# Optimization experiments

Measured on AMD Instinct MI355X. Metric: run time of the kernel, lower is better.

The kernel has to match this reference:

```python
import jax, jax.numpy as jnp
import numpy as np


def axisangle2mat(p):
    # p: [N, 6] = (rotation vector rx,ry,rz, translation tx,ty,tz) -> [N, 3, 4]
    v = p[:, :3]
    t = p[:, 3:]
    theta = jnp.sqrt(jnp.sum(v * v, axis=-1) + 1e-12)  # [N]
    k = v / theta[:, None]
    kx, ky, kz = k[:, 0], k[:, 1], k[:, 2]
    zero = jnp.zeros_like(kx)
    K = jnp.stack([
        jnp.stack([zero, -kz, ky], -1),
        jnp.stack([kz, zero, -kx], -1),
        jnp.stack([-ky, kx, zero], -1),
    ], -2)  # [N,3,3]
    I = jnp.eye(3, dtype=p.dtype)
    s = jnp.sin(theta)[:, None, None]
    c = (1.0 - jnp.cos(theta))[:, None, None]
    R = I + s * K + c * jnp.matmul(K, K)
    return jnp.concatenate([R, t[:, :, None]], axis=-1)  # [N,3,4]


def grid_sample_3d(vol, grid):
    # vol: [D,H,W]; grid: [...,3] with last dim (x,y,z) in [-1,1].
    # Replicates F.grid_sample(mode='bilinear', padding_mode='zeros', align_corners=False).
    D, H, W = vol.shape
    ix = ((grid[..., 0] + 1.0) * W - 1.0) * 0.5
    iy = ((grid[..., 1] + 1.0) * H - 1.0) * 0.5
    iz = ((grid[..., 2] + 1.0) * D - 1.0) * 0.5
    x0 = jnp.floor(ix); y0 = jnp.floor(iy); z0 = jnp.floor(iz)
    fx = ix - x0; fy = iy - y0; fz = iz - z0
    vol_flat = vol.reshape(-1)
    out = jnp.zeros(grid.shape[:-1], vol.dtype)
    for dz in (0, 1):
        for dy in (0, 1):
            for dx in (0, 1):
                xc = x0 + dx; yc = y0 + dy; zc = z0 + dz
                wgt = ((fx if dx else 1.0 - fx) * (fy if dy else 1.0 - fy) * (fz if dz else 1.0 - fz))
                valid = ((xc >= 0) & (xc < W) & (yc >= 0) & (yc < H) & (zc >= 0) & (zc < D))
                xi = jnp.clip(xc, 0, W - 1).astype(jnp.int32)
                yi = jnp.clip(yc, 0, H - 1).astype(jnp.int32)
                zi = jnp.clip(zc, 0, D - 1).astype(jnp.int32)
                v = vol_flat[(zi * H + yi) * W + xi]
                out = out + jnp.where(valid, v * wgt, 0.0)
    return out


def setup_inputs() -> dict:
    key = jax.random.key(0)
    ks = jax.random.split(key, 8)
    B, n, D, H, W = 4096, 2048, 256, 256, 256
    x = jax.random.normal(ks[0], (1, 1, D, H, W), dtype=jnp.float32)
    # voxel-space sample points inside the volume
    sampleGrid = jax.random.uniform(ks[1], (B, 3), dtype=jnp.float32) * jnp.array([W - 1, H - 1, D - 1], jnp.float32)
    ax = jnp.concatenate([
        jax.random.normal(ks[2], (B, 1, 3), dtype=jnp.float32) * 0.1,   # small rotations
        jax.random.normal(ks[3], (B, 1, 3), dtype=jnp.float32) * 5.0,   # translations (voxels)
    ], axis=-1)
    low = jax.random.uniform(ks[4], (B, 1, 3), dtype=jnp.float32) * 2.0
    ext = jax.random.uniform(ks[5], (B, 1, 3), dtype=jnp.float32) * 4.0 + 1.0
    bound = jnp.concatenate([low, low + ext], axis=1)  # [B,2,3], bound[:,1] > bound[:,0]
    A = jax.random.normal(ks[6], (B, 3, 3), dtype=jnp.float32) * 0.3
    InvCovScaled = jnp.einsum('bij,bkj->bik', A, A) + 0.5 * jnp.eye(3, dtype=jnp.float32)  # SPD
    xyz_psf = jax.random.normal(ks[7], (B, n, 3), dtype=jnp.float32)
    psf_sigma = jnp.ones((1,), jnp.float32)  # unused in forward (as in the original)
    return dict(x=x, sampleGrid=sampleGrid, ax=ax, bound=bound,
                InvCovScaled=InvCovScaled, psf_sigma=psf_sigma, xyz_psf=xyz_psf)


def reference(x, sampleGrid, ax, bound, InvCovScaled, psf_sigma, xyz_psf):
    # x: [1,1,D,H,W]; sampleGrid: [B,3]; ax: [B,1,6]; bound: [B,2,3];
    # InvCovScaled: [B,3,3]; xyz_psf: [B,n,3] (the torch.randn draw, made explicit)
    W = x.shape[-1]; H = x.shape[-2]; D = x.shape[-3]
    size = (W, H, D)  # matches torch: size = [x.shape[-1], x.shape[-2], x.shape[-3]]
    scaled_xyz_psf = 2.0 * jax.nn.sigmoid(xyz_psf) - 1.0                      # [B,n,3]
    half = (bound[:, 1, :] - bound[:, 0, :]) * 0.5                            # [B,3]
    bound_psf = scaled_xyz_psf * half[:, None]                                # [B,n,3]
    mat = axisangle2mat(ax.reshape(-1, 6)).reshape(ax.shape[:-1] + (3, 4))    # [B,1,3,4]
    R = mat[:, 0, :, :3]                                                      # [B,3,3]
    T = mat[:, 0, :, 3]                                                       # [B,3]
    # trans_first=True: R @ (p + T)
    mat_sampleGrid = jnp.einsum('bij,bj->bi', R, sampleGrid + T)[:, None]     # [B,1,3]
    psf_sampleGrid = mat_sampleGrid + bound_psf                               # [B,n,3]
    norm = jnp.array([size[0] - 1, size[1] - 1, size[2] - 1], psf_sampleGrid.dtype)
    grid = 2.0 * (psf_sampleGrid / norm - 0.5)
    psf_x = grid_sample_3d(x[0, 0], grid)                                     # [B,n]
    # Mahalanobis-style weights: exp(-0.5 * c^T InvCov c)
    q = jnp.einsum('bni,bij,bnj->bn', bound_psf, InvCovScaled, bound_psf)
    w = jnp.exp(-0.5 * q)                                                     # [B,n]
    y = jnp.sum(psf_x * w, axis=-1) / jnp.sum(w, axis=-1)                     # [B]
    return y
```

## Files before the change

kernel.cpp:

```cpp
#include <hip/hip_runtime.h>
#include <math.h>

constexpr int NT   = 256;
constexpr int WPB  = 4;
constexpr int DIMV = 256;
constexpr int RS   = 8;
constexpr int RROW = 9;
constexpr int RSLICE = RS * RROW;

__device__ __forceinline__ float rflf(float x) {
    return __uint_as_float(__builtin_amdgcn_readfirstlane(__float_as_uint(x)));
}
__device__ __forceinline__ float fexp2(float x) {
#if __has_builtin(__builtin_amdgcn_exp2f)
    return __builtin_amdgcn_exp2f(x);
#else
    return __expf(x * 0.6931471805599453f);
#endif
}

__global__ __launch_bounds__(NT, 4) void psf_sample_kernel(
    const float* __restrict__ vol,
    const float* __restrict__ sampleGrid,
    const float* __restrict__ ax,
    const float* __restrict__ bound,
    const float* __restrict__ invcov,
    const float* __restrict__ xyz,
    float* __restrict__ out,
    int n, int B)
{
    const int tid  = threadIdx.x;
    const int wid  = tid >> 6;
    const int lane = tid & 63;
    const int b    = blockIdx.x * WPB + wid;
    const bool valid = b < B;

    __shared__ float s_vol[WPB][RS * RSLICE];

    const float LOG2E = 1.4426950408889634f;
    float cix, ciy, ciz, hx, hy, hz, addrC;
    float Bxx, Byy, Bzz, Bxy, Bxz, Byz;
    int bx = 0, by = 0, bz = 0;
    bool fast = false;
    float h0 = 0, h1 = 0, h2 = 0;

    if (valid) {
        const float v0 = ax[b*6+0], v1 = ax[b*6+1], v2 = ax[b*6+2];
        const float t0 = ax[b*6+3], t1 = ax[b*6+4], t2 = ax[b*6+5];
        const float theta = sqrtf(v0*v0 + v1*v1 + v2*v2 + 1e-12f);
        const float inv = 1.0f / theta;
        const float kx = v0*inv, ky = v1*inv, kz = v2*inv;
        const float sn = sinf(theta);
        const float cn = 1.0f - cosf(theta);
        const float R00 = 1.0f - cn*(ky*ky + kz*kz);
        const float R01 = -sn*kz + cn*kx*ky;
        const float R02 =  sn*ky + cn*kx*kz;
        const float R10 =  sn*kz + cn*kx*ky;
        const float R11 = 1.0f - cn*(kx*kx + kz*kz);
        const float R12 = -sn*kx + cn*ky*kz;
        const float R20 = -sn*ky + cn*kx*kz;
        const float R21 =  sn*kx + cn*ky*kz;
        const float R22 = 1.0f - cn*(kx*kx + ky*ky);
        const float g0 = sampleGrid[b*3+0] + t0;
        const float g1 = sampleGrid[b*3+1] + t1;
        const float g2 = sampleGrid[b*3+2] + t2;
        const float ms0 = R00*g0 + R01*g1 + R02*g2;
        const float ms1 = R10*g0 + R11*g1 + R12*g2;
        const float ms2 = R20*g0 + R21*g1 + R22*g2;
        h0 = (bound[b*6+3] - bound[b*6+0]) * 0.5f;
        h1 = (bound[b*6+4] - bound[b*6+1]) * 0.5f;
        h2 = (bound[b*6+5] - bound[b*6+2]) * 0.5f;
        const float M00 = invcov[b*9+0], M01 = invcov[b*9+1], M02 = invcov[b*9+2];
        const float M11 = invcov[b*9+4], M12 = invcov[b*9+5], M22 = invcov[b*9+8];

        Bxx = rflf(-0.5f * M00 * h0 * h0 * LOG2E);
        Byy = rflf(-0.5f * M11 * h1 * h1 * LOG2E);
        Bzz = rflf(-0.5f * M22 * h2 * h2 * LOG2E);
        Bxy = rflf(-M01 * h0 * h1 * LOG2E);
        Bxz = rflf(-M02 * h0 * h2 * LOG2E);
        Byz = rflf(-M12 * h1 * h2 * LOG2E);

        const float kk = 256.0f / 255.0f;
        cix = rflf(fmaf(ms0, kk, -0.5f));
        ciy = rflf(fmaf(ms1, kk, -0.5f));
        ciz = rflf(fmaf(ms2, kk, -0.5f));
        hx  = rflf(h0 * kk);
        hy  = rflf(h1 * kk);
        hz  = rflf(h2 * kk);

        bx = __builtin_amdgcn_readfirstlane((int)floorf(cix - hx - 1e-3f));
        by = __builtin_amdgcn_readfirstlane((int)floorf(ciy - hy - 1e-3f));
        bz = __builtin_amdgcn_readfirstlane((int)floorf(ciz - hz - 1e-3f));
        addrC = rflf((float)(bz * RSLICE + by * RROW + bx));
        fast = (hx <= 2.9f) && (hy <= 2.9f) && (hz <= 2.9f);

        if (fast) {
            #pragma unroll
            for (int pass = 0; pass < (RS*RS*RS)/64; ++pass) {
                const int idx = pass * 64 + lane;
                const int lx = idx & 7, ly = (idx >> 3) & 7, lz = idx >> 6;
                const int gx = bx + lx, gy = by + ly, gz = bz + lz;
                float v = 0.0f;
                if ((unsigned)gx < (unsigned)DIMV && (unsigned)gy < (unsigned)DIMV &&
                    (unsigned)gz < (unsigned)DIMV)
                    v = vol[((size_t)gz * DIMV + gy) * DIMV + gx];
                s_vol[wid][(lz * RS + ly) * RROW + lx] = v;
            }
        }
    }
    __syncthreads();

    if (valid) {
        float sum_wx = 0.0f, sum_w = 0.0f;
        const float* __restrict__ sreg = s_vol[wid];

        auto doSample = [&](float rx, float ry, float rz) {
            const float ex = fexp2(rx * -LOG2E);
            const float ey = fexp2(ry * -LOG2E);
            const float ez = fexp2(rz * -LOG2E);
            const float sx = (1.0f - ex) * __builtin_amdgcn_rcpf(1.0f + ex);
            const float sy = (1.0f - ey) * __builtin_amdgcn_rcpf(1.0f + ey);
            const float sz = (1.0f - ez) * __builtin_amdgcn_rcpf(1.0f + ez);

            const float ixf = fmaf(sx, hx, cix);
            const float iyf = fmaf(sy, hy, ciy);
            const float izf = fmaf(sz, hz, ciz);
            const float x0f = floorf(ixf), y0f = floorf(iyf), z0f = floorf(izf);
            const float fx = ixf - x0f, fy = iyf - y0f, fz = izf - z0f;

            float val;
            if (fast) {
                const float ef = fmaf(z0f, (float)RSLICE,
                                 fmaf(y0f, (float)RROW, x0f - addrC));
                const int e = (int)ef;
                const float* p = &sreg[e];
                const float v000 = p[0],              v001 = p[1];
                const float v010 = p[RROW],           v011 = p[RROW + 1];
                const float v100 = p[RSLICE],         v101 = p[RSLICE + 1];
                const float v110 = p[RSLICE + RROW],  v111 = p[RSLICE + RROW + 1];
                const float a00 = fmaf(fx, v001 - v000, v000);
                const float a01 = fmaf(fx, v011 - v010, v010);
                const float a10 = fmaf(fx, v101 - v100, v100);
                const float a11 = fmaf(fx, v111 - v110, v110);
                const float a0  = fmaf(fy, a01 - a00, a00);
                const float a1  = fmaf(fy, a11 - a10, a10);
                val = fmaf(fz, a1 - a0, a0);
            } else {
                const int x0 = (int)x0f, y0 = (int)y0f, z0 = (int)z0f;
                const int x1 = x0 + 1, y1 = y0 + 1, z1 = z0 + 1;
                const bool vx0 = (unsigned)x0 < (unsigned)DIMV;
                const bool vx1 = (unsigned)x1 < (unsigned)DIMV;
                const bool vy0 = (unsigned)y0 < (unsigned)DIMV;
                const bool vy1 = (unsigned)y1 < (unsigned)DIMV;
                const bool vz0 = (unsigned)z0 < (unsigned)DIMV;
                const bool vz1 = (unsigned)z1 < (unsigned)DIMV;
                const int cx0 = min(max(x0,0),DIMV-1), cx1 = min(max(x1,0),DIMV-1);
                const int cy0 = min(max(y0,0),DIMV-1), cy1 = min(max(y1,0),DIMV-1);
                const int cz0 = min(max(z0,0),DIMV-1), cz1 = min(max(z1,0),DIMV-1);
                const float wx0 = 1.0f-fx, wx1 = fx, wy0 = 1.0f-fy, wy1 = fy;
                const float wz0 = 1.0f-fz, wz1 = fz;
                const int r00 = (cz0*DIMV + cy0)*DIMV, r01 = (cz0*DIMV + cy1)*DIMV;
                const int r10 = (cz1*DIMV + cy0)*DIMV, r11 = (cz1*DIMV + cy1)*DIMV;
                val  = (vz0&&vy0&&vx0) ? vol[r00+cx0]*(wz0*wy0*wx0) : 0.0f;
                val += (vz0&&vy0&&vx1) ? vol[r00+cx1]*(wz0*wy0*wx1) : 0.0f;
                val += (vz0&&vy1&&vx0) ? vol[r01+cx0]*(wz0*wy1*wx0) : 0.0f;
                val += (vz0&&vy1&&vx1) ? vol[r01+cx1]*(wz0*wy1*wx1) : 0.0f;
                val += (vz1&&vy0&&vx0) ? vol[r10+cx0]*(wz1*wy0*wx0) : 0.0f;
                val += (vz1&&vy0&&vx1) ? vol[r10+cx1]*(wz1*wy0*wx1) : 0.0f;
                val += (vz1&&vy1&&vx0) ? vol[r11+cx0]*(wz1*wy1*wx0) : 0.0f;
                val += (vz1&&vy1&&vx1) ? vol[r11+cx1]*(wz1*wy1*wx1) : 0.0f;
            }

            const float f = fmaf(Bxx, sx*sx,
                            fmaf(Byy, sy*sy,
                            fmaf(Bzz, sz*sz,
                            fmaf(Bxy, sx*sy,
                            fmaf(Bxz, sx*sz, Byz * (sy*sz))))));
            const float w = fexp2(f);
            sum_w  += w;
            sum_wx = fmaf(w, val, sum_wx);
        };

        const int ng = n >> 2;
        const float4* __restrict__ xb4 =
            reinterpret_cast<const float4*>(xyz + (size_t)b * n * 3);
        for (int g = lane; g < ng; g += 64) {
            const float4 q0 = xb4[g*3 + 0];
            const float4 q1 = xb4[g*3 + 1];
            const float4 q2 = xb4[g*3 + 2];
            doSample(q0.x, q0.y, q0.z);
            doSample(q0.w, q1.x, q1.y);
            doSample(q1.z, q1.w, q2.x);
            doSample(q2.y, q2.z, q2.w);
        }
        const float* __restrict__ xb = xyz + (size_t)b * n * 3;
        for (int i = (ng << 2) + lane; i < n; i += 64)
            doSample(xb[i*3+0], xb[i*3+1], xb[i*3+2]);

        #pragma unroll
        for (int off = 32; off > 0; off >>= 1) {
            sum_wx += __shfl_down(sum_wx, off);
            sum_w  += __shfl_down(sum_w,  off);
        }
        if (lane == 0) out[b] = sum_wx / sum_w;
    }
}

extern "C" void kernel_launch(void* const* d_in, const int* in_sizes, int n_in,
                              void* d_out, int out_size, void* d_ws, size_t ws_size,
                              hipStream_t stream) {
    const float* vol        = (const float*)d_in[0];
    const float* sampleGrid = (const float*)d_in[1];
    const float* ax         = (const float*)d_in[2];
    const float* bound      = (const float*)d_in[3];
    const float* invcov     = (const float*)d_in[4];
    const float* xyz        = (const float*)d_in[6];
    float* out              = (float*)d_out;

    const int B = in_sizes[1] / 3;
    const int n = in_sizes[6] / (B * 3);

    const int grid = (B + WPB - 1) / WPB;
    psf_sample_kernel<<<grid, NT, 0, stream>>>(vol, sampleGrid, ax, bound,
                                               invcov, xyz, out, n, B);
}
```

Baseline: 29.15 us.

## Split each batch item across two waves and store float4 corner quads in LDS

Result: slower. 29.76 us (+2.1%).

```diff
diff --git a/kernel.cpp b/kernel.cpp
--- a/kernel.cpp
+++ b/kernel.cpp
@@ -2,11 +2,10 @@
 #include <math.h>
 
 constexpr int NT   = 256;
-constexpr int WPB  = 4;
 constexpr int DIMV = 256;
 constexpr int RS   = 8;
-constexpr int RROW = 9;
-constexpr int RSLICE = RS * RROW;
+constexpr int QROW = 9;
+constexpr int QSLICE = RS * QROW;
 
 __device__ __forceinline__ float rflf(float x) {
     return __uint_as_float(__builtin_amdgcn_readfirstlane(__float_as_uint(x)));
@@ -19,7 +18,7 @@
 #endif
 }
 
-__global__ __launch_bounds__(NT, 4) void psf_sample_kernel(
+__global__ __launch_bounds__(NT, 8) void psf_sample_kernel(
     const float* __restrict__ vol,
     const float* __restrict__ sampleGrid,
     const float* __restrict__ ax,
@@ -32,17 +31,18 @@
     const int tid  = threadIdx.x;
     const int wid  = tid >> 6;
     const int lane = tid & 63;
-    const int b    = blockIdx.x * WPB + wid;
+    const int pb   = wid >> 1;
+    const int sw   = wid & 1;
+    const int b    = blockIdx.x * 2 + pb;
     const bool valid = b < B;
 
-    __shared__ float s_vol[WPB][RS * RSLICE];
+    __shared__ float4 s_q[2][RS * QSLICE];
+    __shared__ float  s_red[8];
 
     const float LOG2E = 1.4426950408889634f;
-    float cix, ciy, ciz, hx, hy, hz, addrC;
-    float Bxx, Byy, Bzz, Bxy, Bxz, Byz;
-    int bx = 0, by = 0, bz = 0;
+    float cix = 0, ciy = 0, ciz = 0, hx = 0, hy = 0, hz = 0, addrC = 0;
+    float Bxx = 0, Byy = 0, Bzz = 0, Bxy = 0, Bxz = 0, Byz = 0;
     bool fast = false;
-    float h0 = 0, h1 = 0, h2 = 0;
 
     if (valid) {
         const float v0 = ax[b*6+0], v1 = ax[b*6+1], v2 = ax[b*6+2];
@@ -67,9 +67,9 @@
         const float ms0 = R00*g0 + R01*g1 + R02*g2;
         const float ms1 = R10*g0 + R11*g1 + R12*g2;
         const float ms2 = R20*g0 + R21*g1 + R22*g2;
-        h0 = (bound[b*6+3] - bound[b*6+0]) * 0.5f;
-        h1 = (bound[b*6+4] - bound[b*6+1]) * 0.5f;
-        h2 = (bound[b*6+5] - bound[b*6+2]) * 0.5f;
+        const float h0 = (bound[b*6+3] - bound[b*6+0]) * 0.5f;
+        const float h1 = (bound[b*6+4] - bound[b*6+1]) * 0.5f;
+        const float h2 = (bound[b*6+5] - bound[b*6+2]) * 0.5f;
         const float M00 = invcov[b*9+0], M01 = invcov[b*9+1], M02 = invcov[b*9+2];
         const float M11 = invcov[b*9+4], M12 = invcov[b*9+5], M22 = invcov[b*9+8];
 
@@ -88,31 +88,35 @@
         hy  = rflf(h1 * kk);
         hz  = rflf(h2 * kk);
 
-        bx = __builtin_amdgcn_readfirstlane((int)floorf(cix - hx - 1e-3f));
-        by = __builtin_amdgcn_readfirstlane((int)floorf(ciy - hy - 1e-3f));
-        bz = __builtin_amdgcn_readfirstlane((int)floorf(ciz - hz - 1e-3f));
-        addrC = rflf((float)(bz * RSLICE + by * RROW + bx));
+        const int bx = __builtin_amdgcn_readfirstlane((int)floorf(cix - hx - 1e-3f));
+        const int by = __builtin_amdgcn_readfirstlane((int)floorf(ciy - hy - 1e-3f));
+        const int bz = __builtin_amdgcn_readfirstlane((int)floorf(ciz - hz - 1e-3f));
+        addrC = rflf((float)(bz * QSLICE + by * QROW + bx));
         fast = (hx <= 2.9f) && (hy <= 2.9f) && (hz <= 2.9f);
 
         if (fast) {
+            const int lx = lane & 7, ly = lane >> 3;
             #pragma unroll
-            for (int pass = 0; pass < (RS*RS*RS)/64; ++pass) {
-                const int idx = pass * 64 + lane;
-                const int lx = idx & 7, ly = (idx >> 3) & 7, lz = idx >> 6;
-                const int gx = bx + lx, gy = by + ly, gz = bz + lz;
+            for (int p = 0; p < 4; ++p) {
+                const int z  = sw * 4 + p;
+                const int gx = bx + lx, gy = by + ly, gz = bz + z;
                 float v = 0.0f;
                 if ((unsigned)gx < (unsigned)DIMV && (unsigned)gy < (unsigned)DIMV &&
                     (unsigned)gz < (unsigned)DIMV)
                     v = vol[((size_t)gz * DIMV + gy) * DIMV + gx];
-                s_vol[wid][(lz * RS + ly) * RROW + lx] = v;
+                const float v10 = __shfl(v, (lane + 1) & 63);
+                const float v01 = __shfl(v, (lane + 8) & 63);
+                const float v11 = __shfl(v, (lane + 9) & 63);
+                s_q[pb][(z * RS + ly) * QROW + lx] = make_float4(v, v10, v01, v11);
             }
         }
     }
     __syncthreads();
 
+    float sum_wx = 0.0f, sum_w = 0.0f;
+
     if (valid) {
-        float sum_wx = 0.0f, sum_w = 0.0f;
-        const float* __restrict__ sreg = s_vol[wid];
+        const float4* __restrict__ sreg = s_q[pb];
 
         auto doSample = [&](float rx, float ry, float rz) {
             const float ex = fexp2(rx * -LOG2E);
@@ -130,19 +134,16 @@
 
             float val;
             if (fast) {
-                const float ef = fmaf(z0f, (float)RSLICE,
-                                 fmaf(y0f, (float)RROW, x0f - addrC));
+                const float ef = fmaf(z0f, (float)QSLICE,
+                                 fmaf(y0f, (float)QROW, x0f - addrC));
                 const int e = (int)ef;
-                const float* p = &sreg[e];
-                const float v000 = p[0],              v001 = p[1];
-                const float v010 = p[RROW],           v011 = p[RROW + 1];
-                const float v100 = p[RSLICE],         v101 = p[RSLICE + 1];
-                const float v110 = p[RSLICE + RROW],  v111 = p[RSLICE + RROW + 1];
-                const float a00 = fmaf(fx, v001 - v000, v000);
-                const float a01 = fmaf(fx, v011 - v010, v010);
-                const float a10 = fmaf(fx, v101 - v100, v100);
-                const float a11 = fmaf(fx, v111 - v110, v110);
+                const float4 q0 = sreg[e];
+                const float4 q1 = sreg[e + QSLICE];
+                const float a00 = fmaf(fx, q0.y - q0.x, q0.x);
+                const float a01 = fmaf(fx, q0.w - q0.z, q0.z);
                 const float a0  = fmaf(fy, a01 - a00, a00);
+                const float a10 = fmaf(fx, q1.y - q1.x, q1.x);
+                const float a11 = fmaf(fx, q1.w - q1.z, q1.z);
                 const float a1  = fmaf(fy, a11 - a10, a10);
                 val = fmaf(fz, a1 - a0, a0);
             } else {
@@ -184,7 +185,7 @@
         const int ng = n >> 2;
         const float4* __restrict__ xb4 =
             reinterpret_cast<const float4*>(xyz + (size_t)b * n * 3);
-        for (int g = lane; g < ng; g += 64) {
+        for (int g = lane + 64 * sw; g < ng; g += 128) {
             const float4 q0 = xb4[g*3 + 0];
             const float4 q1 = xb4[g*3 + 1];
             const float4 q2 = xb4[g*3 + 2];
@@ -194,7 +195,7 @@
             doSample(q2.y, q2.z, q2.w);
         }
         const float* __restrict__ xb = xyz + (size_t)b * n * 3;
-        for (int i = (ng << 2) + lane; i < n; i += 64)
+        for (int i = (ng << 2) + lane + 64 * sw; i < n; i += 128)
             doSample(xb[i*3+0], xb[i*3+1], xb[i*3+2]);
 
         #pragma unroll
@@ -202,7 +203,14 @@
             sum_wx += __shfl_down(sum_wx, off);
             sum_w  += __shfl_down(sum_w,  off);
         }
-        if (lane == 0) out[b] = sum_wx / sum_w;
+        if (lane == 0) { s_red[wid*2] = sum_wx; s_red[wid*2+1] = sum_w; }
+    }
+    __syncthreads();
+
+    if (valid && lane == 0 && sw == 0) {
+        const float twx = s_red[wid*2] + s_red[(wid+1)*2];
+        const float tw  = s_red[wid*2+1] + s_red[(wid+1)*2+1];
+        out[b] = twx / tw;
     }
 }
 
@@ -220,7 +228,7 @@
     const int B = in_sizes[1] / 3;
     const int n = in_sizes[6] / (B * 3);
 
-    const int grid = (B + WPB - 1) / WPB;
+    const int grid = (B + 1) / 2;
     psf_sample_kernel<<<grid, NT, 0, stream>>>(vol, sampleGrid, ax, bound,
                                                invcov, xyz, out, n, B);
 }
```
